# Performance work log

Measured on AMD Instinct MI355X. Metric: run time of the kernel, lower is better.

## Reference

```python
import jax, jax.numpy as jnp
import numpy as np

LMAX = 5
L = LMAX + 1            # L_out = L_in = 6
DIM = L * L             # 36 spherical-harmonic coefficients
RES_B = 2 * L           # 12 beta points (Gauss-Legendre in cos(beta))
RES_A = 2 * L           # 12 alpha points (uniform)
CORRELATION = 3
REPEATS = np.arange(1, 2 * L, 2)  # [1,3,5,7,9,11]: ir.dim per l, mul=1 in irreps_out


def _normalized_assoc_legendre(lmax, x):
    """Fully (L2 on sphere) normalized associated Legendre Pbar_l^m(x), no CS phase.
    Returns dict[(l,m)] -> np.ndarray over x."""
    P = {}
    s = np.sqrt(np.maximum(1.0 - x * x, 0.0))
    P[(0, 0)] = np.full_like(x, np.sqrt(1.0 / (4.0 * np.pi)))
    for m in range(1, lmax + 1):
        P[(m, m)] = np.sqrt((2.0 * m + 1.0) / (2.0 * m)) * s * P[(m - 1, m - 1)]
    for m in range(0, lmax):
        P[(m + 1, m)] = np.sqrt(2.0 * m + 3.0) * x * P[(m, m)]
    for m in range(0, lmax + 1):
        for l in range(m + 2, lmax + 1):
            a = np.sqrt((4.0 * l * l - 1.0) / (l * l - m * m))
            b = np.sqrt(((l - 1.0) ** 2 - m * m) / (4.0 * (l - 1.0) ** 2 - 1.0))
            P[(l, m)] = a * (x * P[(l - 1, m)] - b * P[(l - 2, m)])
    return P


def build_s2grid(lmax, res_beta, res_alpha):
    """Y: [res_beta, res_alpha, (lmax+1)^2] real orthonormal SH samples.
    Yw: Y with quadrature weights so that einsum(f, Yw) inverts einsum(c, Y)."""
    xq, wq = np.polynomial.legendre.leggauss(res_beta)  # nodes in cos(beta)
    alpha = np.arange(res_alpha) * (2.0 * np.pi / res_alpha)
    P = _normalized_assoc_legendre(lmax, xq)
    dim = (lmax + 1) ** 2
    Y = np.zeros((res_beta, res_alpha, dim))
    sqrt2 = np.sqrt(2.0)
    for l in range(lmax + 1):
        for m in range(-l, l + 1):
            idx = l * l + l + m
            plm = P[(l, abs(m))]
            if m > 0:
                ang = sqrt2 * np.cos(m * alpha)
            elif m == 0:
                ang = np.ones(res_alpha)
            else:
                ang = sqrt2 * np.sin(-m * alpha)
            Y[:, :, idx] = plm[:, None] * ang[None, :]
    Yw = Y * wq[:, None, None] * (2.0 * np.pi / res_alpha)
    return jnp.asarray(Y, jnp.float32), jnp.asarray(Yw, jnp.float32)


def setup_inputs() -> dict:
    key = jax.random.key(0)
    k1, k2, k3 = jax.random.split(key, 3)
    atom_feat = jax.random.normal(k1, (4096, 128, DIM), dtype=jnp.float32)
    atom_type = jax.random.uniform(k2, (4096, 10), dtype=jnp.float32)
    weights = jax.random.normal(k3, (CORRELATION, 10, 128, L), dtype=jnp.float32)
    return {"atom_feat": atom_feat, "atom_type": atom_type, "weights": weights}


def reference(atom_feat, atom_type, weights):
    Y, Yw = build_s2grid(LMAX, RES_B, RES_A)

    def to_grid(c):      # [n, C, DIM] -> [n, C, beta, alpha]
        return jnp.einsum('nck,bak->ncba', c, Y)

    def from_grid(f):    # [n, C, beta, alpha] -> [n, C, DIM]
        return jnp.einsum('ncba,bak->nck', f, Yw)

    def apply_w(w):      # w: [E, C, L]; atom-type-weighted, expanded to DIM
        wn = jnp.einsum('ne,ecl->ncl', atom_type, w)  # [n, C, L]
        return jnp.repeat(wn, REPEATS, axis=-1, total_repeat_length=DIM)

    feat_grid = to_grid(atom_feat)  # reused across correlation orders
    prod = atom_feat
    result = apply_w(weights[0]) * prod
    for nu in range(1, CORRELATION):
        # Gaunt tensor product via S2 grid: pointwise multiply on the sphere
        prod = from_grid(to_grid(prod) * feat_grid)
        result = result + apply_w(weights[nu]) * prod
    return jnp.squeeze(result)
```

## Files before the change

kernel.cpp:

```cpp
#include <hip/hip_runtime.h>

namespace tabs {

constexpr double PI_ = 3.14159265358979323846;

constexpr double csqrt(double x) {
  double g = x > 1.0 ? x : 1.0;
  for (int i = 0; i < 48; ++i) g = 0.5 * (g + x / g);
  return g;
}
constexpr double ccos(double x) {
  double x2 = x * x, t = 1.0, s = 1.0;
  for (int k = 1; k <= 20; ++k) { t *= -x2 / ((2.0 * k - 1.0) * (2.0 * k)); s += t; }
  return s;
}
constexpr double csin(double x) {
  double x2 = x * x, t = x, s = x;
  for (int k = 1; k <= 20; ++k) { t *= -x2 / ((2.0 * k) * (2.0 * k + 1.0)); s += t; }
  return s;
}

struct GL { double x[12]; double w[12]; };

constexpr GL gl12() {
  GL g{};
  for (int i = 0; i < 12; ++i) {
    double x = ccos(PI_ * (i + 0.75) / 12.5);
    for (int it = 0; it < 50; ++it) {
      double p0 = 1.0, p1 = x;
      for (int k = 2; k <= 12; ++k) { double pk = ((2.0 * k - 1.0) * x * p1 - (k - 1.0) * p0) / k; p0 = p1; p1 = pk; }
      double dp = 12.0 * (x * p1 - p0) / (x * x - 1.0);
      x -= p1 / dp;
    }
    double p0 = 1.0, p1 = x;
    for (int k = 2; k <= 12; ++k) { double pk = ((2.0 * k - 1.0) * x * p1 - (k - 1.0) * p0) / k; p0 = p1; p1 = pk; }
    double dp = 12.0 * (x * p1 - p0) / (x * x - 1.0);
    g.x[i] = x;
    g.w[i] = 2.0 / ((1.0 - x * x) * dp * dp);
  }
  return g;
}

struct Tables {
  float PA[12][36];
  float PB[12][36];
  float CT[12][6];
  float ST[12][6];
  int   M5[36];
  int   LK[36];
};

constexpr Tables make() {
  Tables t{};
  GL g = gl12();
  for (int b = 0; b < 12; ++b) {
    double x = g.x[b];
    double s = csqrt(1.0 - x * x);
    double P[6][6] = {};
    P[0][0] = csqrt(1.0 / (4.0 * PI_));
    for (int m = 1; m <= 5; ++m) P[m][m] = csqrt((2.0 * m + 1.0) / (2.0 * m)) * s * P[m - 1][m - 1];
    for (int m = 0; m < 5; ++m)  P[m + 1][m] = csqrt(2.0 * m + 3.0) * x * P[m][m];
    for (int m = 0; m <= 5; ++m)
      for (int l = m + 2; l <= 5; ++l) {
        double aa = csqrt((4.0 * l * l - 1.0) / (double)(l * l - m * m));
        double bb = csqrt(((l - 1.0) * (l - 1.0) - (double)(m * m)) / (4.0 * (l - 1.0) * (l - 1.0) - 1.0));
        P[l][m] = aa * (x * P[l - 1][m] - bb * P[l - 2][m]);
      }
    for (int l = 0; l <= 5; ++l)
      for (int m = -l; m <= l; ++m) {
        int k = l * l + l + m, am = m < 0 ? -m : m;
        t.PA[b][k] = (float)P[l][am];
        t.PB[b][k] = (float)(P[l][am] * g.w[b] * (2.0 * PI_ / 12.0));
      }
  }
  double r2 = csqrt(2.0);
  for (int a = 0; a < 12; ++a) {
    t.CT[a][0] = 1.0f; t.ST[a][0] = 0.0f;
    for (int m = 1; m <= 5; ++m) {
      int q = (m * a) % 12;
      double ang = 2.0 * PI_ * q / 12.0;
      if (ang > PI_) ang -= 2.0 * PI_;
      t.CT[a][m] = (float)(r2 * ccos(ang));
      t.ST[a][m] = (float)(r2 * csin(ang));
    }
  }
  for (int l = 0; l <= 5; ++l)
    for (int m = -l; m <= l; ++m) { int k = l * l + l + m; t.M5[k] = m + 5; t.LK[k] = l; }
  return t;
}

}

__device__ constexpr tabs::Tables T = tabs::make();

__device__ __forceinline__ unsigned bf16rn(float x) {
  unsigned u = __float_as_uint(x);
  return (u + 0x7FFFu + ((u >> 16) & 1u)) >> 16;
}

__global__ __launch_bounds__(128, 2)
void gaunt_s2_kernel(const float* __restrict__ feat,
                     const float* __restrict__ atype,
                     const float* __restrict__ wts,
                     float* __restrict__ out) {
  __shared__ unsigned fsh[72][128];

  const int tid = threadIdx.x;
  const int atom = blockIdx.x;
  const size_t row = (size_t)atom * 128 + tid;

  float c0[36];
  {
    const float4* p = reinterpret_cast<const float4*>(feat + row * 36);
#pragma unroll
    for (int i = 0; i < 9; ++i) {
      float4 v = p[i];
      c0[4 * i + 0] = v.x; c0[4 * i + 1] = v.y; c0[4 * i + 2] = v.z; c0[4 * i + 3] = v.w;
    }
  }

  float prod1[36];
#pragma unroll
  for (int k = 0; k < 36; ++k) prod1[k] = 0.f;

  for (int b = 0; b < 12; ++b) {
    float u[11];
#pragma unroll
    for (int i = 0; i < 11; ++i) u[i] = 0.f;
#pragma unroll
    for (int k = 0; k < 36; ++k) u[T.M5[k]] += c0[k] * T.PA[b][k];

    float v[11];
#pragma unroll
    for (int i = 0; i < 11; ++i) v[i] = 0.f;

#pragma unroll
    for (int j = 0; j < 6; ++j) {
      float fpair[2];
#pragma unroll
      for (int h = 0; h < 2; ++h) {
        const int a = 2 * j + h;
        float t = u[5];
#pragma unroll
        for (int m = 1; m <= 5; ++m) {
          t += u[5 + m] * T.CT[a][m];
          t += u[5 - m] * T.ST[a][m];
        }
        fpair[h] = t;
        const float g = t * t;
        v[5] += g;
#pragma unroll
        for (int m = 1; m <= 5; ++m) {
          v[5 + m] += g * T.CT[a][m];
          v[5 - m] += g * T.ST[a][m];
        }
      }
      fsh[b * 6 + j][tid] = bf16rn(fpair[0]) | (bf16rn(fpair[1]) << 16);
    }

#pragma unroll
    for (int k = 0; k < 36; ++k) prod1[k] += v[T.M5[k]] * T.PB[b][k];
  }

  float prod2[36];
#pragma unroll
  for (int k = 0; k < 36; ++k) prod2[k] = 0.f;

  for (int b = 0; b < 12; ++b) {
    float u[11];
#pragma unroll
    for (int i = 0; i < 11; ++i) u[i] = 0.f;
#pragma unroll
    for (int k = 0; k < 36; ++k) u[T.M5[k]] += prod1[k] * T.PA[b][k];

    float v[11];
#pragma unroll
    for (int i = 0; i < 11; ++i) v[i] = 0.f;

#pragma unroll
    for (int j = 0; j < 6; ++j) {
      const unsigned pck = fsh[b * 6 + j][tid];
#pragma unroll
      for (int h = 0; h < 2; ++h) {
        const int a = 2 * j + h;
        float t = u[5];
#pragma unroll
        for (int m = 1; m <= 5; ++m) {
          t += u[5 + m] * T.CT[a][m];
          t += u[5 - m] * T.ST[a][m];
        }
        const float f = __uint_as_float(h == 0 ? (pck << 16) : (pck & 0xFFFF0000u));
        const float g = t * f;
        v[5] += g;
#pragma unroll
        for (int m = 1; m <= 5; ++m) {
          v[5 + m] += g * T.CT[a][m];
          v[5 - m] += g * T.ST[a][m];
        }
      }
    }

#pragma unroll
    for (int k = 0; k < 36; ++k) prod2[k] += v[T.M5[k]] * T.PB[b][k];
  }

  float at10[10];
#pragma unroll
  for (int e = 0; e < 10; ++e) at10[e] = atype[(size_t)atom * 10 + e];

  float wn[3][6];
#pragma unroll
  for (int nu = 0; nu < 3; ++nu)
#pragma unroll
    for (int l = 0; l < 6; ++l) wn[nu][l] = 0.f;

#pragma unroll
  for (int nu = 0; nu < 3; ++nu) {
#pragma unroll
    for (int e = 0; e < 10; ++e) {
      const float* wp = wts + ((size_t)(nu * 10 + e) * 128 + tid) * 6;
#pragma unroll
      for (int l = 0; l < 6; ++l) wn[nu][l] += at10[e] * wp[l];
    }
  }

  float* op = out + row * 36;
#pragma unroll
  for (int i = 0; i < 9; ++i) {
    float4 v;
    {
      const int k = 4 * i + 0, l = T.LK[k];
      v.x = wn[0][l] * c0[k] + wn[1][l] * prod1[k] + wn[2][l] * prod2[k];
    }
    {
      const int k = 4 * i + 1, l = T.LK[k];
      v.y = wn[0][l] * c0[k] + wn[1][l] * prod1[k] + wn[2][l] * prod2[k];
    }
    {
      const int k = 4 * i + 2, l = T.LK[k];
      v.z = wn[0][l] * c0[k] + wn[1][l] * prod1[k] + wn[2][l] * prod2[k];
    }
    {
      const int k = 4 * i + 3, l = T.LK[k];
      v.w = wn[0][l] * c0[k] + wn[1][l] * prod1[k] + wn[2][l] * prod2[k];
    }
    reinterpret_cast<float4*>(op)[i] = v;
  }
}

extern "C" void kernel_launch(void* const* d_in, const int* in_sizes, int n_in,
                              void* d_out, int out_size, void* d_ws, size_t ws_size,
                              hipStream_t stream) {
  const float* feat = (const float*)d_in[0];
  const float* atype = (const float*)d_in[1];
  const float* wts = (const float*)d_in[2];
  float* out = (float*)d_out;

  (void)in_sizes; (void)n_in; (void)out_size; (void)d_ws; (void)ws_size;

  gaunt_s2_kernel<<<4096, 128, 0, stream>>>(feat, atype, wts, out);
}
```

Measured before the change: 267.5 us.

## Replace scalar separable SH transforms with bf16 MFMA dense grid matmuls

The per-thread separable Legendre/Fourier transforms are replaced by dense synthesis (36x144) and analysis (144x36) matrices, precomputed at compile time in bf16 and laid out for MFMA fragments. Each block of 256 threads runs four bf16 16x16x32 MFMA GEMM stages over the block's 128 channels, staging intermediates in shared memory. The pointwise grid products and the final weighted combination are fused in between and at the end. This trades the fp32 VALU work of the factored transform for matrix-core throughput, at the cost of more total FLOPs and bf16 rounding of the input, grid values and intermediate coefficients.

```diff
diff --git a/kernel.cpp b/kernel.cpp
--- a/kernel.cpp
+++ b/kernel.cpp
@@ -1,22 +1,23 @@
 #include <hip/hip_runtime.h>
-
-namespace tabs {
+#include <stdint.h>
+
+namespace ct {
 
 constexpr double PI_ = 3.14159265358979323846;
 
 constexpr double csqrt(double x) {
   double g = x > 1.0 ? x : 1.0;
-  for (int i = 0; i < 48; ++i) g = 0.5 * (g + x / g);
+  for (int i = 0; i < 40; ++i) g = 0.5 * (g + x / g);
   return g;
 }
 constexpr double ccos(double x) {
   double x2 = x * x, t = 1.0, s = 1.0;
-  for (int k = 1; k <= 20; ++k) { t *= -x2 / ((2.0 * k - 1.0) * (2.0 * k)); s += t; }
+  for (int k = 1; k <= 16; ++k) { t *= -x2 / ((2.0 * k - 1.0) * (2.0 * k)); s += t; }
   return s;
 }
 constexpr double csin(double x) {
   double x2 = x * x, t = x, s = x;
-  for (int k = 1; k <= 20; ++k) { t *= -x2 / ((2.0 * k) * (2.0 * k + 1.0)); s += t; }
+  for (int k = 1; k <= 16; ++k) { t *= -x2 / ((2.0 * k) * (2.0 * k + 1.0)); s += t; }
   return s;
 }
 
@@ -41,17 +42,14 @@
   return g;
 }
 
-struct Tables {
-  float PA[12][36];
-  float PB[12][36];
-  float CT[12][6];
-  float ST[12][6];
-  int   M5[36];
-  int   LK[36];
+struct Tab {
+  double PA[12][36];
+  double PB[12][36];
+  double ANG[12][36];
 };
 
-constexpr Tables make() {
-  Tables t{};
+constexpr Tab make_tab() {
+  Tab t{};
   GL g = gl12();
   for (int b = 0; b < 12; ++b) {
     double x = g.x[b];
@@ -69,183 +67,327 @@
     for (int l = 0; l <= 5; ++l)
       for (int m = -l; m <= l; ++m) {
         int k = l * l + l + m, am = m < 0 ? -m : m;
-        t.PA[b][k] = (float)P[l][am];
-        t.PB[b][k] = (float)(P[l][am] * g.w[b] * (2.0 * PI_ / 12.0));
+        t.PA[b][k] = P[l][am];
+        t.PB[b][k] = P[l][am] * g.w[b] * (2.0 * PI_ / 12.0);
       }
   }
   double r2 = csqrt(2.0);
-  for (int a = 0; a < 12; ++a) {
-    t.CT[a][0] = 1.0f; t.ST[a][0] = 0.0f;
-    for (int m = 1; m <= 5; ++m) {
-      int q = (m * a) % 12;
-      double ang = 2.0 * PI_ * q / 12.0;
-      if (ang > PI_) ang -= 2.0 * PI_;
-      t.CT[a][m] = (float)(r2 * ccos(ang));
-      t.ST[a][m] = (float)(r2 * csin(ang));
-    }
-  }
-  for (int l = 0; l <= 5; ++l)
-    for (int m = -l; m <= l; ++m) { int k = l * l + l + m; t.M5[k] = m + 5; t.LK[k] = l; }
+  for (int a = 0; a < 12; ++a)
+    for (int l = 0; l <= 5; ++l)
+      for (int m = -l; m <= l; ++m) {
+        int k = l * l + l + m, am = m < 0 ? -m : m;
+        double v = 1.0;
+        if (m != 0) {
+          int qq = (am * a) % 12;
+          double ang = 2.0 * PI_ * qq / 12.0;
+          if (ang > PI_) ang -= 2.0 * PI_;
+          v = (m > 0) ? r2 * ccos(ang) : r2 * csin(ang);
+        }
+        t.ANG[a][k] = v;
+      }
   return t;
 }
 
-}
-
-__device__ constexpr tabs::Tables T = tabs::make();
-
-__device__ __forceinline__ unsigned bf16rn(float x) {
-  unsigned u = __float_as_uint(x);
-  return (u + 0x7FFFu + ((u >> 16) & 1u)) >> 16;
-}
-
-__global__ __launch_bounds__(128, 2)
-void gaunt_s2_kernel(const float* __restrict__ feat,
-                     const float* __restrict__ atype,
-                     const float* __restrict__ wts,
-                     float* __restrict__ out) {
-  __shared__ unsigned fsh[72][128];
+constexpr Tab TD = make_tab();
+
+constexpr unsigned f2bf(double x) {
+  if (x == 0.0) return 0u;
+  unsigned s = 0u; double a = x;
+  if (a < 0.0) { s = 0x8000u; a = -a; }
+  int e = 127;
+  while (a >= 2.0) { a *= 0.5; ++e; }
+  while (a < 1.0)  { a *= 2.0; --e; }
+  double md = (a - 1.0) * 128.0;
+  int mi = (int)md;
+  double fr = md - mi;
+  if (fr > 0.5 || (fr == 0.5 && (mi & 1))) ++mi;
+  if (mi == 128) { mi = 0; ++e; }
+  return s | ((unsigned)e << 7) | (unsigned)mi;
+}
+
+constexpr double syn_val(int k, int n) {
+  if (k >= 36 || n >= 144) return 0.0;
+  int b = n / 12, a = n % 12;
+  return TD.PA[b][k] * TD.ANG[a][k];
+}
+constexpr double ana_val(int kp, int np) {
+  if (kp >= 144 || np >= 36) return 0.0;
+  int b = kp / 12, a = kp % 12;
+  return TD.PB[b][np] * TD.ANG[a][np];
+}
+
+struct alignas(16) SynArr { unsigned v[2 * 10 * 64 * 4]; };
+struct alignas(16) AnaArr { unsigned v[5 * 3 * 64 * 4]; };
+
+constexpr SynArr make_syn() {
+  SynArr F{};
+  for (int ks = 0; ks < 2; ++ks)
+    for (int nt = 0; nt < 10; ++nt)
+      for (int lane = 0; lane < 64; ++lane)
+        for (int jp = 0; jp < 4; ++jp) {
+          int q = lane >> 4, l16 = lane & 15;
+          int k0 = ks * 32 + q * 8 + jp * 2;
+          int n = nt * 16 + l16;
+          F.v[((ks * 10 + nt) * 64 + lane) * 4 + jp] =
+              f2bf(syn_val(k0, n)) | (f2bf(syn_val(k0 + 1, n)) << 16);
+        }
+  return F;
+}
+constexpr AnaArr make_ana() {
+  AnaArr F{};
+  for (int ks = 0; ks < 5; ++ks)
+    for (int nt = 0; nt < 3; ++nt)
+      for (int lane = 0; lane < 64; ++lane)
+        for (int jp = 0; jp < 4; ++jp) {
+          int q = lane >> 4, l16 = lane & 15;
+          int k0 = ks * 32 + q * 8 + jp * 2;
+          int n = nt * 16 + l16;
+          F.v[((ks * 3 + nt) * 64 + lane) * 4 + jp] =
+              f2bf(ana_val(k0, n)) | (f2bf(ana_val(k0 + 1, n)) << 16);
+        }
+  return F;
+}
+
+}
+
+__device__ constexpr ct::SynArr SYNB = ct::make_syn();
+__device__ constexpr ct::AnaArr ANAB = ct::make_ana();
+
+typedef __attribute__((ext_vector_type(8))) short short8;
+typedef __attribute__((ext_vector_type(4))) float f32x4;
+
+#define STRC 80
+#define STRG 168
+
+__device__ __forceinline__ unsigned short bfr(float x) {
+  return (unsigned short)((__float_as_uint(x) + 0x8000u) >> 16);
+}
+__device__ __forceinline__ float bf2f(unsigned short u) {
+  return __uint_as_float(((unsigned)u) << 16);
+}
+constexpr int lk(int k) { return k >= 25 ? 5 : k >= 16 ? 4 : k >= 9 ? 3 : k >= 4 ? 2 : k >= 1 ? 1 : 0; }
+
+template <int KB>
+__device__ __forceinline__ void epilogue_half(int r, const float* fp, float* op,
+                                              const unsigned short* CO, const float* Gf,
+                                              const float wn0[6], const float wn1[6], const float wn2[6]) {
+#pragma unroll
+  for (int p = 0; p < 9; ++p) {
+    const int k0 = KB + 2 * p, k1 = k0 + 1;
+    const int l0 = lk(k0), l1 = lk(k1);
+    float2 c0v = *reinterpret_cast<const float2*>(fp + 2 * p);
+    float2 p2v = *reinterpret_cast<const float2*>(&Gf[r * 40 + k0]);
+    float p10 = bf2f(CO[r * STRC + k0]);
+    float p11 = bf2f(CO[r * STRC + k1]);
+    float2 o;
+    o.x = wn0[l0] * c0v.x + wn1[l0] * p10 + wn2[l0] * p2v.x;
+    o.y = wn0[l1] * c0v.y + wn1[l1] * p11 + wn2[l1] * p2v.y;
+    *reinterpret_cast<float2*>(op + 2 * p) = o;
+  }
+}
+
+__global__ __launch_bounds__(256, 2)
+void gaunt_mfma_kernel(const float* __restrict__ feat,
+                       const float* __restrict__ atype,
+                       const float* __restrict__ wts,
+                       float* __restrict__ out) {
+  __shared__ unsigned short CO[128 * STRC];
+  __shared__ unsigned short G[128 * STRG];
+  float* Gf = reinterpret_cast<float*>(G);
 
   const int tid = threadIdx.x;
   const int atom = blockIdx.x;
-  const size_t row = (size_t)atom * 128 + tid;
-
-  float c0[36];
-  {
-    const float4* p = reinterpret_cast<const float4*>(feat + row * 36);
-#pragma unroll
-    for (int i = 0; i < 9; ++i) {
-      float4 v = p[i];
-      c0[4 * i + 0] = v.x; c0[4 * i + 1] = v.y; c0[4 * i + 2] = v.z; c0[4 * i + 3] = v.w;
-    }
-  }
-
-  float prod1[36];
-#pragma unroll
-  for (int k = 0; k < 36; ++k) prod1[k] = 0.f;
-
-  for (int b = 0; b < 12; ++b) {
-    float u[11];
-#pragma unroll
-    for (int i = 0; i < 11; ++i) u[i] = 0.f;
-#pragma unroll
-    for (int k = 0; k < 36; ++k) u[T.M5[k]] += c0[k] * T.PA[b][k];
-
-    float v[11];
-#pragma unroll
-    for (int i = 0; i < 11; ++i) v[i] = 0.f;
-
-#pragma unroll
-    for (int j = 0; j < 6; ++j) {
-      float fpair[2];
-#pragma unroll
-      for (int h = 0; h < 2; ++h) {
-        const int a = 2 * j + h;
-        float t = u[5];
-#pragma unroll
-        for (int m = 1; m <= 5; ++m) {
-          t += u[5 + m] * T.CT[a][m];
-          t += u[5 - m] * T.ST[a][m];
-        }
-        fpair[h] = t;
-        const float g = t * t;
-        v[5] += g;
-#pragma unroll
-        for (int m = 1; m <= 5; ++m) {
-          v[5 + m] += g * T.CT[a][m];
-          v[5 - m] += g * T.ST[a][m];
-        }
+  const int w = tid >> 6, lane = tid & 63, q = lane >> 4, l16 = lane & 15;
+  const size_t fbase = (size_t)atom * 4608;
+
+#pragma unroll
+  for (int it = 0; it < 18; ++it) {
+    int i = tid + 256 * it;
+    int row = i / 36, col = i - row * 36;
+    CO[row * STRC + col] = bfr(feat[fbase + i]);
+  }
+#pragma unroll
+  for (int it = 0; it < 14; ++it) {
+    int j = tid + 256 * it;
+    int row = j / 28, col = 36 + (j - row * 28);
+    CO[row * STRC + col] = 0;
+  }
+  __syncthreads();
+
+  f32x4 accA[2][10];
+#pragma unroll
+  for (int mi = 0; mi < 2; ++mi)
+#pragma unroll
+    for (int nt = 0; nt < 10; ++nt) accA[mi][nt] = f32x4{0.f, 0.f, 0.f, 0.f};
+
+#pragma unroll
+  for (int ks = 0; ks < 2; ++ks) {
+    short8 af[2];
+#pragma unroll
+    for (int mi = 0; mi < 2; ++mi)
+      af[mi] = *reinterpret_cast<const short8*>(&CO[((2 * w + mi) * 16 + l16) * STRC + ks * 32 + q * 8]);
+#pragma unroll
+    for (int nt = 0; nt < 10; ++nt) {
+      short8 bf = *reinterpret_cast<const short8*>(&SYNB.v[((ks * 10 + nt) * 64 + lane) * 4]);
+      accA[0][nt] = __builtin_amdgcn_mfma_f32_16x16x32_bf16(af[0], bf, accA[0][nt], 0, 0, 0);
+      accA[1][nt] = __builtin_amdgcn_mfma_f32_16x16x32_bf16(af[1], bf, accA[1][nt], 0, 0, 0);
+    }
+  }
+
+  unsigned fpk[2][10][2];
+#pragma unroll
+  for (int mi = 0; mi < 2; ++mi)
+#pragma unroll
+    for (int nt = 0; nt < 10; ++nt) {
+      f32x4 v = accA[mi][nt];
+      const int r0 = (2 * w + mi) * 16 + q * 4;
+      const int col = nt * 16 + l16;
+      unsigned b0 = bfr(v.x), b1 = bfr(v.y), b2 = bfr(v.z), b3 = bfr(v.w);
+      fpk[mi][nt][0] = b0 | (b1 << 16);
+      fpk[mi][nt][1] = b2 | (b3 << 16);
+      G[(r0 + 0) * STRG + col] = bfr(v.x * v.x);
+      G[(r0 + 1) * STRG + col] = bfr(v.y * v.y);
+      G[(r0 + 2) * STRG + col] = bfr(v.z * v.z);
+      G[(r0 + 3) * STRG + col] = bfr(v.w * v.w);
+    }
+  __syncthreads();
+
+  f32x4 acc2[2][3];
+#pragma unroll
+  for (int mi = 0; mi < 2; ++mi)
+#pragma unroll
+    for (int nt = 0; nt < 3; ++nt) acc2[mi][nt] = f32x4{0.f, 0.f, 0.f, 0.f};
+
+#pragma unroll
+  for (int ks = 0; ks < 5; ++ks) {
+    short8 ga[2];
+#pragma unroll
+    for (int mi = 0; mi < 2; ++mi)
+      ga[mi] = *reinterpret_cast<const short8*>(&G[((2 * w + mi) * 16 + l16) * STRG + ks * 32 + q * 8]);
+#pragma unroll
+    for (int nt = 0; nt < 3; ++nt) {
+      short8 bf = *reinterpret_cast<const short8*>(&ANAB.v[((ks * 3 + nt) * 64 + lane) * 4]);
+      acc2[0][nt] = __builtin_amdgcn_mfma_f32_16x16x32_bf16(ga[0], bf, acc2[0][nt], 0, 0, 0);
+      acc2[1][nt] = __builtin_amdgcn_mfma_f32_16x16x32_bf16(ga[1], bf, acc2[1][nt], 0, 0, 0);
+    }
+  }
+
+#pragma unroll
+  for (int mi = 0; mi < 2; ++mi)
+#pragma unroll
+    for (int nt = 0; nt < 3; ++nt) {
+      f32x4 v = acc2[mi][nt];
+      const int r0 = (2 * w + mi) * 16 + q * 4;
+      const int col = nt * 16 + l16;
+      CO[(r0 + 0) * STRC + col] = bfr(v.x);
+      CO[(r0 + 1) * STRC + col] = bfr(v.y);
+      CO[(r0 + 2) * STRC + col] = bfr(v.z);
+      CO[(r0 + 3) * STRC + col] = bfr(v.w);
+    }
+  __syncthreads();
+
+  f32x4 acc3[2][10];
+#pragma unroll
+  for (int mi = 0; mi < 2; ++mi)
+#pragma unroll
+    for (int nt = 0; nt < 10; ++nt) acc3[mi][nt] = f32x4{0.f, 0.f, 0.f, 0.f};
+
+#pragma unroll
+  for (int ks = 0; ks < 2; ++ks) {
+    short8 af[2];
+#pragma unroll
+    for (int mi = 0; mi < 2; ++mi)
+      af[mi] = *reinterpret_cast<const short8*>(&CO[((2 * w + mi) * 16 + l16) * STRC + ks * 32 + q * 8]);
+#pragma unroll
+    for (int nt = 0; nt < 10; ++nt) {
+      short8 bf = *reinterpret_cast<const short8*>(&SYNB.v[((ks * 10 + nt) * 64 + lane) * 4]);
+      acc3[0][nt] = __builtin_amdgcn_mfma_f32_16x16x32_bf16(af[0], bf, acc3[0][nt], 0, 0, 0);
+      acc3[1][nt] = __builtin_amdgcn_mfma_f32_16x16x32_bf16(af[1], bf, acc3[1][nt], 0, 0, 0);
+    }
+  }
+
+#pragma unroll
+  for (int mi = 0; mi < 2; ++mi)
+#pragma unroll
+    for (int nt = 0; nt < 10; ++nt) {
+      f32x4 v = acc3[mi][nt];
+      const int r0 = (2 * w + mi) * 16 + q * 4;
+      const int col = nt * 16 + l16;
+      float f0 = __uint_as_float(fpk[mi][nt][0] << 16);
+      float f1 = __uint_as_float(fpk[mi][nt][0] & 0xFFFF0000u);
+      float f2_ = __uint_as_float(fpk[mi][nt][1] << 16);
+      float f3 = __uint_as_float(fpk[mi][nt][1] & 0xFFFF0000u);
+      G[(r0 + 0) * STRG + col] = bfr(v.x * f0);
+      G[(r0 + 1) * STRG + col] = bfr(v.y * f1);
+      G[(r0 + 2) * STRG + col] = bfr(v.z * f2_);
+      G[(r0 + 3) * STRG + col] = bfr(v.w * f3);
+    }
+  __syncthreads();
+
+  f32x4 acc4[2][3];
+#pragma unroll
+  for (int mi = 0; mi < 2; ++mi)
+#pragma unroll
+    for (int nt = 0; nt < 3; ++nt) acc4[mi][nt] = f32x4{0.f, 0.f, 0.f, 0.f};
+
+#pragma unroll
+  for (int ks = 0; ks < 5; ++ks) {
+    short8 ga[2];
+#pragma unroll
+    for (int mi = 0; mi < 2; ++mi)
+      ga[mi] = *reinterpret_cast<const short8*>(&G[((2 * w + mi) * 16 + l16) * STRG + ks * 32 + q * 8]);
+#pragma unroll
+    for (int nt = 0; nt < 3; ++nt) {
+      short8 bf = *reinterpret_cast<const short8*>(&ANAB.v[((ks * 3 + nt) * 64 + lane) * 4]);
+      acc4[0][nt] = __builtin_amdgcn_mfma_f32_16x16x32_bf16(ga[0], bf, acc4[0][nt], 0, 0, 0);
+      acc4[1][nt] = __builtin_amdgcn_mfma_f32_16x16x32_bf16(ga[1], bf, acc4[1][nt], 0, 0, 0);
+    }
+  }
+  __syncthreads();
+
+#pragma unroll
+  for (int mi = 0; mi < 2; ++mi)
+#pragma unroll
+    for (int nt = 0; nt < 3; ++nt) {
+      const int col = nt * 16 + l16;
+      if (col < 36) {
+        f32x4 v = acc4[mi][nt];
+        const int r0 = (2 * w + mi) * 16 + q * 4;
+        Gf[(r0 + 0) * 40 + col] = v.x;
+        Gf[(r0 + 1) * 40 + col] = v.y;
+        Gf[(r0 + 2) * 40 + col] = v.z;
+        Gf[(r0 + 3) * 40 + col] = v.w;
       }
-      fsh[b * 6 + j][tid] = bf16rn(fpair[0]) | (bf16rn(fpair[1]) << 16);
-    }
-
-#pragma unroll
-    for (int k = 0; k < 36; ++k) prod1[k] += v[T.M5[k]] * T.PB[b][k];
-  }
-
-  float prod2[36];
-#pragma unroll
-  for (int k = 0; k < 36; ++k) prod2[k] = 0.f;
-
-  for (int b = 0; b < 12; ++b) {
-    float u[11];
-#pragma unroll
-    for (int i = 0; i < 11; ++i) u[i] = 0.f;
-#pragma unroll
-    for (int k = 0; k < 36; ++k) u[T.M5[k]] += prod1[k] * T.PA[b][k];
-
-    float v[11];
-#pragma unroll
-    for (int i = 0; i < 11; ++i) v[i] = 0.f;
-
-#pragma unroll
-    for (int j = 0; j < 6; ++j) {
-      const unsigned pck = fsh[b * 6 + j][tid];
-#pragma unroll
-      for (int h = 0; h < 2; ++h) {
-        const int a = 2 * j + h;
-        float t = u[5];
-#pragma unroll
-        for (int m = 1; m <= 5; ++m) {
-          t += u[5 + m] * T.CT[a][m];
-          t += u[5 - m] * T.ST[a][m];
-        }
-        const float f = __uint_as_float(h == 0 ? (pck << 16) : (pck & 0xFFFF0000u));
-        const float g = t * f;
-        v[5] += g;
-#pragma unroll
-        for (int m = 1; m <= 5; ++m) {
-          v[5 + m] += g * T.CT[a][m];
-          v[5 - m] += g * T.ST[a][m];
-        }
-      }
-    }
-
-#pragma unroll
-    for (int k = 0; k < 36; ++k) prod2[k] += v[T.M5[k]] * T.PB[b][k];
-  }
-
-  float at10[10];
-#pragma unroll
-  for (int e = 0; e < 10; ++e) at10[e] = atype[(size_t)atom * 10 + e];
-
-  float wn[3][6];
-#pragma unroll
-  for (int nu = 0; nu < 3; ++nu)
-#pragma unroll
-    for (int l = 0; l < 6; ++l) wn[nu][l] = 0.f;
-
-#pragma unroll
-  for (int nu = 0; nu < 3; ++nu) {
-#pragma unroll
-    for (int e = 0; e < 10; ++e) {
-      const float* wp = wts + ((size_t)(nu * 10 + e) * 128 + tid) * 6;
-#pragma unroll
-      for (int l = 0; l < 6; ++l) wn[nu][l] += at10[e] * wp[l];
-    }
-  }
-
-  float* op = out + row * 36;
-#pragma unroll
-  for (int i = 0; i < 9; ++i) {
-    float4 v;
-    {
-      const int k = 4 * i + 0, l = T.LK[k];
-      v.x = wn[0][l] * c0[k] + wn[1][l] * prod1[k] + wn[2][l] * prod2[k];
-    }
-    {
-      const int k = 4 * i + 1, l = T.LK[k];
-      v.y = wn[0][l] * c0[k] + wn[1][l] * prod1[k] + wn[2][l] * prod2[k];
-    }
-    {
-      const int k = 4 * i + 2, l = T.LK[k];
-      v.z = wn[0][l] * c0[k] + wn[1][l] * prod1[k] + wn[2][l] * prod2[k];
-    }
-    {
-      const int k = 4 * i + 3, l = T.LK[k];
-      v.w = wn[0][l] * c0[k] + wn[1][l] * prod1[k] + wn[2][l] * prod2[k];
-    }
-    reinterpret_cast<float4*>(op)[i] = v;
-  }
+    }
+  __syncthreads();
+
+  const int half = tid >> 7;
+  const int r = tid & 127;
+
+  float at[10];
+#pragma unroll
+  for (int e = 0; e < 10; ++e) at[e] = atype[atom * 10 + e];
+
+  float wn0[6], wn1[6], wn2[6];
+#pragma unroll
+  for (int l = 0; l < 6; ++l) { wn0[l] = 0.f; wn1[l] = 0.f; wn2[l] = 0.f; }
+#pragma unroll
+  for (int e = 0; e < 10; ++e) {
+    const float* w0p = wts + ((size_t)(0 * 10 + e) * 128 + r) * 6;
+    const float* w1p = wts + ((size_t)(1 * 10 + e) * 128 + r) * 6;
+    const float* w2p = wts + ((size_t)(2 * 10 + e) * 128 + r) * 6;
+#pragma unroll
+    for (int l = 0; l < 6; ++l) {
+      wn0[l] += at[e] * w0p[l];
+      wn1[l] += at[e] * w1p[l];
+      wn2[l] += at[e] * w2p[l];
+    }
+  }
+
+  const float* fp = feat + fbase + (size_t)r * 36 + half * 18;
+  float* op = out + fbase + (size_t)r * 36 + half * 18;
+  if (half == 0) epilogue_half<0>(r, fp, op, CO, Gf, wn0, wn1, wn2);
+  else           epilogue_half<18>(r, fp, op, CO, Gf, wn0, wn1, wn2);
 }
 
 extern "C" void kernel_launch(void* const* d_in, const int* in_sizes, int n_in,
@@ -255,8 +397,7 @@
   const float* atype = (const float*)d_in[1];
   const float* wts = (const float*)d_in[2];
   float* out = (float*)d_out;
-
   (void)in_sizes; (void)n_in; (void)out_size; (void)d_ws; (void)ws_size;
 
-  gaunt_s2_kernel<<<4096, 128, 0, stream>>>(feat, atype, wts, out);
-}
+  gaunt_mfma_kernel<<<4096, 256, 0, stream>>>(feat, atype, wts, out);
+}
```

Result: slower. 293.0 us (+9.5%).

## Recast S2 grid transforms as bf16 MFMA matmuls with constexpr basis tables

Applied to the files above, without the earlier changes.

Replaces the per-thread scalar spherical-harmonic synthesis/analysis loops with dense bf16 matrix multiplies on MFMA 32x32x16. Each wavefront takes a 32-row tile of (atom, channel) pairs and multiplies by precomputed 36x144 synthesis and 144x36 analysis matrices stored in lane-swizzled layout. Grid values and intermediate coefficients go through LDS in bf16. The FMA-heavy scalar work moves onto matrix cores, at the cost of padding (144 to 160, 36 to 48), bf16 rounding of the coefficients and basis values, and uncoalesced scalar output stores.

```diff
diff --git a/kernel.cpp b/kernel.cpp
--- a/kernel.cpp
+++ b/kernel.cpp
@@ -1,22 +1,23 @@
 #include <hip/hip_runtime.h>
-
-namespace tabs {
+#include <stdint.h>
+
+namespace ct {
 
 constexpr double PI_ = 3.14159265358979323846;
 
 constexpr double csqrt(double x) {
   double g = x > 1.0 ? x : 1.0;
-  for (int i = 0; i < 48; ++i) g = 0.5 * (g + x / g);
+  for (int i = 0; i < 40; ++i) g = 0.5 * (g + x / g);
   return g;
 }
 constexpr double ccos(double x) {
   double x2 = x * x, t = 1.0, s = 1.0;
-  for (int k = 1; k <= 20; ++k) { t *= -x2 / ((2.0 * k - 1.0) * (2.0 * k)); s += t; }
+  for (int k = 1; k <= 16; ++k) { t *= -x2 / ((2.0 * k - 1.0) * (2.0 * k)); s += t; }
   return s;
 }
 constexpr double csin(double x) {
   double x2 = x * x, t = x, s = x;
-  for (int k = 1; k <= 20; ++k) { t *= -x2 / ((2.0 * k) * (2.0 * k + 1.0)); s += t; }
+  for (int k = 1; k <= 16; ++k) { t *= -x2 / ((2.0 * k) * (2.0 * k + 1.0)); s += t; }
   return s;
 }
 
@@ -41,17 +42,14 @@
   return g;
 }
 
-struct Tables {
-  float PA[12][36];
-  float PB[12][36];
-  float CT[12][6];
-  float ST[12][6];
-  int   M5[36];
-  int   LK[36];
+struct Tab {
+  double PA[12][36];
+  double PB[12][36];
+  double ANG[12][36];
 };
 
-constexpr Tables make() {
-  Tables t{};
+constexpr Tab make_tab() {
+  Tab t{};
   GL g = gl12();
   for (int b = 0; b < 12; ++b) {
     double x = g.x[b];
@@ -69,182 +67,296 @@
     for (int l = 0; l <= 5; ++l)
       for (int m = -l; m <= l; ++m) {
         int k = l * l + l + m, am = m < 0 ? -m : m;
-        t.PA[b][k] = (float)P[l][am];
-        t.PB[b][k] = (float)(P[l][am] * g.w[b] * (2.0 * PI_ / 12.0));
+        t.PA[b][k] = P[l][am];
+        t.PB[b][k] = P[l][am] * g.w[b] * (2.0 * PI_ / 12.0);
       }
   }
   double r2 = csqrt(2.0);
-  for (int a = 0; a < 12; ++a) {
-    t.CT[a][0] = 1.0f; t.ST[a][0] = 0.0f;
-    for (int m = 1; m <= 5; ++m) {
-      int q = (m * a) % 12;
-      double ang = 2.0 * PI_ * q / 12.0;
-      if (ang > PI_) ang -= 2.0 * PI_;
-      t.CT[a][m] = (float)(r2 * ccos(ang));
-      t.ST[a][m] = (float)(r2 * csin(ang));
-    }
-  }
-  for (int l = 0; l <= 5; ++l)
-    for (int m = -l; m <= l; ++m) { int k = l * l + l + m; t.M5[k] = m + 5; t.LK[k] = l; }
+  for (int a = 0; a < 12; ++a)
+    for (int l = 0; l <= 5; ++l)
+      for (int m = -l; m <= l; ++m) {
+        int k = l * l + l + m, am = m < 0 ? -m : m;
+        double v = 1.0;
+        if (m != 0) {
+          int qq = (am * a) % 12;
+          double ang = 2.0 * PI_ * qq / 12.0;
+          if (ang > PI_) ang -= 2.0 * PI_;
+          v = (m > 0) ? r2 * ccos(ang) : r2 * csin(ang);
+        }
+        t.ANG[a][k] = v;
+      }
   return t;
 }
 
-}
-
-__device__ constexpr tabs::Tables T = tabs::make();
-
-__device__ __forceinline__ unsigned bf16rn(float x) {
-  unsigned u = __float_as_uint(x);
-  return (u + 0x7FFFu + ((u >> 16) & 1u)) >> 16;
-}
+constexpr Tab TD = make_tab();
+
+constexpr unsigned f2bf(double x) {
+  if (x == 0.0) return 0u;
+  unsigned s = 0u; double a = x;
+  if (a < 0.0) { s = 0x8000u; a = -a; }
+  int e = 127;
+  while (a >= 2.0) { a *= 0.5; ++e; }
+  while (a < 1.0)  { a *= 2.0; --e; }
+  double md = (a - 1.0) * 128.0;
+  int mi = (int)md;
+  double fr = md - mi;
+  if (fr > 0.5 || (fr == 0.5 && (mi & 1))) ++mi;
+  if (mi == 128) { mi = 0; ++e; }
+  return s | ((unsigned)e << 7) | (unsigned)mi;
+}
+
+constexpr double syn_val(int k, int n) {
+  if (k >= 36 || n >= 144) return 0.0;
+  int b = n / 12, a = n % 12;
+  return TD.PA[b][k] * TD.ANG[a][k];
+}
+constexpr double ana_val(int kp, int np) {
+  if (kp >= 144 || np >= 36) return 0.0;
+  int b = kp / 12, a = kp % 12;
+  return TD.PB[b][np] * TD.ANG[a][np];
+}
+
+struct alignas(16) Syn32 { unsigned v[3 * 5 * 64 * 4]; };
+struct alignas(16) Ana32 { unsigned v[9 * 2 * 64 * 4]; };
+
+constexpr Syn32 make_syn32() {
+  Syn32 F{};
+  for (int ks = 0; ks < 3; ++ks)
+    for (int nt = 0; nt < 5; ++nt)
+      for (int lane = 0; lane < 64; ++lane)
+        for (int jp = 0; jp < 4; ++jp) {
+          int h = lane >> 5, n = nt * 32 + (lane & 31);
+          int k0 = ks * 16 + h * 8 + jp * 2;
+          F.v[((ks * 5 + nt) * 64 + lane) * 4 + jp] =
+              f2bf(syn_val(k0, n)) | (f2bf(syn_val(k0 + 1, n)) << 16);
+        }
+  return F;
+}
+constexpr Ana32 make_ana32() {
+  Ana32 F{};
+  for (int ks = 0; ks < 9; ++ks)
+    for (int nt = 0; nt < 2; ++nt)
+      for (int lane = 0; lane < 64; ++lane)
+        for (int jp = 0; jp < 4; ++jp) {
+          int h = lane >> 5, n = nt * 32 + (lane & 31);
+          int k0 = ks * 16 + h * 8 + jp * 2;
+          F.v[((ks * 2 + nt) * 64 + lane) * 4 + jp] =
+              f2bf(ana_val(k0, n)) | (f2bf(ana_val(k0 + 1, n)) << 16);
+        }
+  return F;
+}
+
+}
+
+__device__ constexpr ct::Syn32 SYNB = ct::make_syn32();
+__device__ constexpr ct::Ana32 ANAB = ct::make_ana32();
+
+typedef __attribute__((ext_vector_type(8))) short short8;
+typedef __attribute__((ext_vector_type(16))) float f32x16;
+
+union S8 { short8 s; unsigned u[4]; uint2 u2[2]; };
+
+__device__ __forceinline__ unsigned short bfr(float x) {
+  return (unsigned short)((__float_as_uint(x) + 0x8000u) >> 16);
+}
+__device__ __forceinline__ unsigned pk2(float x, float y) {
+  return (unsigned)bfr(x) | ((unsigned)bfr(y) << 16);
+}
+__device__ __forceinline__ float lo16(unsigned u) { return __uint_as_float(u << 16); }
+__device__ __forceinline__ float hi16(unsigned u) { return __uint_as_float(u & 0xFFFF0000u); }
+
+__device__ __forceinline__ short8 synf(int ks, int nt, int lane) {
+  const uint4* p = reinterpret_cast<const uint4*>(SYNB.v) + (ks * 5 + nt) * 64 + lane;
+  uint4 t = *p; S8 r; r.u[0] = t.x; r.u[1] = t.y; r.u[2] = t.z; r.u[3] = t.w; return r.s;
+}
+__device__ __forceinline__ short8 anaf(int ks, int nt, int lane) {
+  const uint4* p = reinterpret_cast<const uint4*>(ANAB.v) + (ks * 2 + nt) * 64 + lane;
+  uint4 t = *p; S8 r; r.u[0] = t.x; r.u[1] = t.y; r.u[2] = t.z; r.u[3] = t.w; return r.s;
+}
+
+#define FWS 148
+#define COS 52
 
 __global__ __launch_bounds__(128, 2)
-void gaunt_s2_kernel(const float* __restrict__ feat,
-                     const float* __restrict__ atype,
-                     const float* __restrict__ wts,
-                     float* __restrict__ out) {
-  __shared__ unsigned fsh[72][128];
+void gaunt32_kernel(const float* __restrict__ feat,
+                    const float* __restrict__ atype,
+                    const float* __restrict__ wts,
+                    float* __restrict__ out) {
+  __shared__ unsigned short FW[2][32 * FWS];
+  __shared__ unsigned short CO[2][32 * COS];
+  __shared__ float WN[2][18 * 32];
 
   const int tid = threadIdx.x;
-  const int atom = blockIdx.x;
-  const size_t row = (size_t)atom * 128 + tid;
-
-  float c0[36];
-  {
-    const float4* p = reinterpret_cast<const float4*>(feat + row * 36);
-#pragma unroll
-    for (int i = 0; i < 9; ++i) {
-      float4 v = p[i];
-      c0[4 * i + 0] = v.x; c0[4 * i + 1] = v.y; c0[4 * i + 2] = v.z; c0[4 * i + 3] = v.w;
-    }
-  }
-
-  float prod1[36];
-#pragma unroll
-  for (int k = 0; k < 36; ++k) prod1[k] = 0.f;
-
-  for (int b = 0; b < 12; ++b) {
-    float u[11];
-#pragma unroll
-    for (int i = 0; i < 11; ++i) u[i] = 0.f;
-#pragma unroll
-    for (int k = 0; k < 36; ++k) u[T.M5[k]] += c0[k] * T.PA[b][k];
-
-    float v[11];
-#pragma unroll
-    for (int i = 0; i < 11; ++i) v[i] = 0.f;
-
-#pragma unroll
-    for (int j = 0; j < 6; ++j) {
-      float fpair[2];
-#pragma unroll
-      for (int h = 0; h < 2; ++h) {
-        const int a = 2 * j + h;
-        float t = u[5];
-#pragma unroll
-        for (int m = 1; m <= 5; ++m) {
-          t += u[5 + m] * T.CT[a][m];
-          t += u[5 - m] * T.ST[a][m];
-        }
-        fpair[h] = t;
-        const float g = t * t;
-        v[5] += g;
-#pragma unroll
-        for (int m = 1; m <= 5; ++m) {
-          v[5 + m] += g * T.CT[a][m];
-          v[5 - m] += g * T.ST[a][m];
-        }
-      }
-      fsh[b * 6 + j][tid] = bf16rn(fpair[0]) | (bf16rn(fpair[1]) << 16);
-    }
-
-#pragma unroll
-    for (int k = 0; k < 36; ++k) prod1[k] += v[T.M5[k]] * T.PB[b][k];
-  }
-
-  float prod2[36];
-#pragma unroll
-  for (int k = 0; k < 36; ++k) prod2[k] = 0.f;
-
-  for (int b = 0; b < 12; ++b) {
-    float u[11];
-#pragma unroll
-    for (int i = 0; i < 11; ++i) u[i] = 0.f;
-#pragma unroll
-    for (int k = 0; k < 36; ++k) u[T.M5[k]] += prod1[k] * T.PA[b][k];
-
-    float v[11];
-#pragma unroll
-    for (int i = 0; i < 11; ++i) v[i] = 0.f;
-
-#pragma unroll
-    for (int j = 0; j < 6; ++j) {
-      const unsigned pck = fsh[b * 6 + j][tid];
-#pragma unroll
-      for (int h = 0; h < 2; ++h) {
-        const int a = 2 * j + h;
-        float t = u[5];
-#pragma unroll
-        for (int m = 1; m <= 5; ++m) {
-          t += u[5 + m] * T.CT[a][m];
-          t += u[5 - m] * T.ST[a][m];
-        }
-        const float f = __uint_as_float(h == 0 ? (pck << 16) : (pck & 0xFFFF0000u));
-        const float g = t * f;
-        v[5] += g;
-#pragma unroll
-        for (int m = 1; m <= 5; ++m) {
-          v[5 + m] += g * T.CT[a][m];
-          v[5 - m] += g * T.ST[a][m];
-        }
-      }
-    }
-
-#pragma unroll
-    for (int k = 0; k < 36; ++k) prod2[k] += v[T.M5[k]] * T.PB[b][k];
-  }
-
-  float at10[10];
-#pragma unroll
-  for (int e = 0; e < 10; ++e) at10[e] = atype[(size_t)atom * 10 + e];
-
-  float wn[3][6];
-#pragma unroll
-  for (int nu = 0; nu < 3; ++nu)
-#pragma unroll
-    for (int l = 0; l < 6; ++l) wn[nu][l] = 0.f;
-
-#pragma unroll
-  for (int nu = 0; nu < 3; ++nu) {
-#pragma unroll
-    for (int e = 0; e < 10; ++e) {
-      const float* wp = wts + ((size_t)(nu * 10 + e) * 128 + tid) * 6;
-#pragma unroll
-      for (int l = 0; l < 6; ++l) wn[nu][l] += at10[e] * wp[l];
-    }
-  }
-
-  float* op = out + row * 36;
-#pragma unroll
-  for (int i = 0; i < 9; ++i) {
-    float4 v;
-    {
-      const int k = 4 * i + 0, l = T.LK[k];
-      v.x = wn[0][l] * c0[k] + wn[1][l] * prod1[k] + wn[2][l] * prod2[k];
-    }
-    {
-      const int k = 4 * i + 1, l = T.LK[k];
-      v.y = wn[0][l] * c0[k] + wn[1][l] * prod1[k] + wn[2][l] * prod2[k];
-    }
-    {
-      const int k = 4 * i + 2, l = T.LK[k];
-      v.z = wn[0][l] * c0[k] + wn[1][l] * prod1[k] + wn[2][l] * prod2[k];
-    }
-    {
-      const int k = 4 * i + 3, l = T.LK[k];
-      v.w = wn[0][l] * c0[k] + wn[1][l] * prod1[k] + wn[2][l] * prod2[k];
-    }
-    reinterpret_cast<float4*>(op)[i] = v;
+  const int ws = __builtin_amdgcn_readfirstlane(tid >> 6);
+  const int lane = tid & 63;
+  const int m = lane & 31, h = lane >> 5;
+  const int mtile = blockIdx.x * 2 + ws;
+  const int rowbase = mtile * 32;
+  const int atom = mtile >> 2;
+  const int chb = (mtile & 3) * 32;
+
+  unsigned short* fw = FW[ws];
+  unsigned short* co = CO[ws];
+  float* wn = WN[ws];
+
+  const float* fr = feat + (rowbase + m) * 36;
+  S8 af[3];
+  {
+    float4 a = *reinterpret_cast<const float4*>(fr + h * 8);
+    float4 b = *reinterpret_cast<const float4*>(fr + h * 8 + 4);
+    af[0].u[0] = pk2(a.x, a.y); af[0].u[1] = pk2(a.z, a.w);
+    af[0].u[2] = pk2(b.x, b.y); af[0].u[3] = pk2(b.z, b.w);
+    a = *reinterpret_cast<const float4*>(fr + 16 + h * 8);
+    b = *reinterpret_cast<const float4*>(fr + 20 + h * 8);
+    af[1].u[0] = pk2(a.x, a.y); af[1].u[1] = pk2(a.z, a.w);
+    af[1].u[2] = pk2(b.x, b.y); af[1].u[3] = pk2(b.z, b.w);
+    af[2].u[0] = 0; af[2].u[1] = 0; af[2].u[2] = 0; af[2].u[3] = 0;
+    if (h == 0) {
+      a = *reinterpret_cast<const float4*>(fr + 32);
+      af[2].u[0] = pk2(a.x, a.y); af[2].u[1] = pk2(a.z, a.w);
+    }
+  }
+
+  unsigned fpk[5][8];
+#pragma unroll
+  for (int nt = 0; nt < 5; ++nt) {
+    f32x16 acc = {0.f, 0.f, 0.f, 0.f, 0.f, 0.f, 0.f, 0.f,
+                  0.f, 0.f, 0.f, 0.f, 0.f, 0.f, 0.f, 0.f};
+#pragma unroll
+    for (int ks = 0; ks < 3; ++ks)
+      acc = __builtin_amdgcn_mfma_f32_32x32x16_bf16(af[ks].s, synf(ks, nt, lane), acc, 0, 0, 0);
+    const int col = nt * 32 + m;
+#pragma unroll
+    for (int g = 0; g < 4; ++g) {
+      fpk[nt][2 * g + 0] = pk2(acc[4 * g + 0], acc[4 * g + 1]);
+      fpk[nt][2 * g + 1] = pk2(acc[4 * g + 2], acc[4 * g + 3]);
+    }
+    if (col < 144) {
+#pragma unroll
+      for (int g = 0; g < 4; ++g)
+#pragma unroll
+        for (int i = 0; i < 4; ++i) {
+          float v = acc[4 * g + i];
+          fw[(i + 8 * g + 4 * h) * FWS + col] = bfr(v * v);
+        }
+    }
+  }
+
+  S8 ga[9];
+  {
+    const unsigned short* fr2 = &fw[m * FWS + h * 8];
+#pragma unroll
+    for (int ks = 0; ks < 9; ++ks) {
+      ga[ks].u2[0] = *reinterpret_cast<const uint2*>(fr2 + ks * 16);
+      ga[ks].u2[1] = *reinterpret_cast<const uint2*>(fr2 + ks * 16 + 4);
+    }
+  }
+  f32x16 p1[2];
+#pragma unroll
+  for (int nt = 0; nt < 2; ++nt) {
+    f32x16 acc = {0.f, 0.f, 0.f, 0.f, 0.f, 0.f, 0.f, 0.f,
+                  0.f, 0.f, 0.f, 0.f, 0.f, 0.f, 0.f, 0.f};
+#pragma unroll
+    for (int ks = 0; ks < 9; ++ks)
+      acc = __builtin_amdgcn_mfma_f32_32x32x16_bf16(ga[ks].s, anaf(ks, nt, lane), acc, 0, 0, 0);
+    p1[nt] = acc;
+  }
+
+#pragma unroll
+  for (int nt = 0; nt < 2; ++nt) {
+    const int col = nt * 32 + m;
+    if (col < 48) {
+#pragma unroll
+      for (int g = 0; g < 4; ++g)
+#pragma unroll
+        for (int i = 0; i < 4; ++i)
+          co[(i + 8 * g + 4 * h) * COS + col] = bfr(p1[nt][4 * g + i]);
+    }
+  }
+
+  S8 ca[3];
+  {
+    const unsigned short* cr = &co[m * COS + h * 8];
+#pragma unroll
+    for (int ks = 0; ks < 3; ++ks) {
+      ca[ks].u2[0] = *reinterpret_cast<const uint2*>(cr + ks * 16);
+      ca[ks].u2[1] = *reinterpret_cast<const uint2*>(cr + ks * 16 + 4);
+    }
+  }
+#pragma unroll
+  for (int nt = 0; nt < 5; ++nt) {
+    f32x16 acc = {0.f, 0.f, 0.f, 0.f, 0.f, 0.f, 0.f, 0.f,
+                  0.f, 0.f, 0.f, 0.f, 0.f, 0.f, 0.f, 0.f};
+#pragma unroll
+    for (int ks = 0; ks < 3; ++ks)
+      acc = __builtin_amdgcn_mfma_f32_32x32x16_bf16(ca[ks].s, synf(ks, nt, lane), acc, 0, 0, 0);
+    const int col = nt * 32 + m;
+    if (col < 144) {
+#pragma unroll
+      for (int g = 0; g < 4; ++g)
+#pragma unroll
+        for (int i = 0; i < 4; ++i) {
+          unsigned pk = fpk[nt][2 * g + (i >> 1)];
+          float f = (i & 1) ? hi16(pk) : lo16(pk);
+          fw[(i + 8 * g + 4 * h) * FWS + col] = bfr(acc[4 * g + i] * f);
+        }
+    }
+  }
+
+  {
+    const unsigned short* fr2 = &fw[m * FWS + h * 8];
+#pragma unroll
+    for (int ks = 0; ks < 9; ++ks) {
+      ga[ks].u2[0] = *reinterpret_cast<const uint2*>(fr2 + ks * 16);
+      ga[ks].u2[1] = *reinterpret_cast<const uint2*>(fr2 + ks * 16 + 4);
+    }
+  }
+  f32x16 p2[2];
+#pragma unroll
+  for (int nt = 0; nt < 2; ++nt) {
+    f32x16 acc = {0.f, 0.f, 0.f, 0.f, 0.f, 0.f, 0.f, 0.f,
+                  0.f, 0.f, 0.f, 0.f, 0.f, 0.f, 0.f, 0.f};
+#pragma unroll
+    for (int ks = 0; ks < 9; ++ks)
+      acc = __builtin_amdgcn_mfma_f32_32x32x16_bf16(ga[ks].s, anaf(ks, nt, lane), acc, 0, 0, 0);
+    p2[nt] = acc;
+  }
+
+  {
+    float at[10];
+#pragma unroll
+    for (int e = 0; e < 10; ++e) at[e] = atype[atom * 10 + e];
+#pragma unroll
+    for (int t = 0; t < 9; ++t) {
+      const int p = h + 2 * t;
+      const int nu = p >= 12 ? 2 : (p >= 6 ? 1 : 0);
+      const int l = p - nu * 6;
+      const float* wb = wts + ((nu * 10) * 128 + chb + m) * 6 + l;
+      float s = 0.f;
+#pragma unroll
+      for (int e = 0; e < 10; ++e) s += at[e] * wb[e * 768];
+      wn[p * 32 + m] = s;
+    }
+  }
+
+#pragma unroll
+  for (int nt = 0; nt < 2; ++nt) {
+    const int col = nt * 32 + m;
+    if (col < 36) {
+      const int lc = col >= 25 ? 5 : col >= 16 ? 4 : col >= 9 ? 3 : col >= 4 ? 2 : col >= 1 ? 1 : 0;
+#pragma unroll
+      for (int g = 0; g < 4; ++g)
+#pragma unroll
+        for (int i = 0; i < 4; ++i) {
+          const int row = i + 8 * g + 4 * h;
+          const float c0 = feat[(rowbase + row) * 36 + col];
+          const float w0 = wn[(lc + 0) * 32 + row];
+          const float w1 = wn[(lc + 6) * 32 + row];
+          const float w2 = wn[(lc + 12) * 32 + row];
+          out[(size_t)(rowbase + row) * 36 + col] =
+              w0 * c0 + w1 * p1[nt][4 * g + i] + w2 * p2[nt][4 * g + i];
+        }
+    }
   }
 }
 
@@ -255,8 +367,7 @@
   const float* atype = (const float*)d_in[1];
   const float* wts = (const float*)d_in[2];
   float* out = (float*)d_out;
-
   (void)in_sizes; (void)n_in; (void)out_size; (void)d_ws; (void)ws_size;
 
-  gaunt_s2_kernel<<<4096, 128, 0, stream>>>(feat, atype, wts, out);
-}
+  gaunt32_kernel<<<8192, 128, 0, stream>>>(feat, atype, wts, out);
+}
```

New measurement: 227.0 us. 15.1% less time.
